# Kernel optimization log

Measured on AMD Instinct MI355X. Metric: run time of the kernel, lower is better.

The kernel has to match this reference:

```python
import jax, jax.numpy as jnp
import numpy as np

NUM_LEVELS = 16
MIN_RES = 16
MAX_RES = 256
LOG2_T = 19
TABLE_SIZE = 1 << LOG2_T
F = 2
N = 262144
HASH_INIT_SCALE = 0.001

# Static constants (mirror the torch buffers)
_PRIMES = np.array([1, 2654435761, 805459861, 3674653429], dtype=np.uint32)
_GROWTH = np.exp((np.log(MAX_RES) - np.log(MIN_RES)) / (NUM_LEVELS - 1))
_SCALINGS = np.floor(MIN_RES * _GROWTH ** np.arange(NUM_LEVELS)).astype(np.float32)  # [L]
_HASH_OFFSET = (np.arange(NUM_LEVELS) * TABLE_SIZE).astype(np.int32)  # [L]
_CORNERS = np.array([[(i >> d) & 1 for d in range(4)] for i in range(16)], dtype=np.int32)  # [16,4]


def setup_inputs() -> dict:
    key = jax.random.key(0)
    k1, k2 = jax.random.split(key)
    xyzt = jax.random.uniform(k1, (N, 4), dtype=jnp.float32)  # coords in [0,1)
    hash_table = (jax.random.uniform(k2, (TABLE_SIZE * NUM_LEVELS, F), dtype=jnp.float32) * 2.0 - 1.0) * HASH_INIT_SCALE
    return {"xyzt": xyzt, "hash_table": hash_table}


def reference(xyzt, hash_table):
    # xyzt: [N,4], hash_table: [L*T, F]
    primes = jnp.asarray(_PRIMES)                      # uint32
    scalings = jnp.asarray(_SCALINGS)                  # [L]
    hash_offset = jnp.asarray(_HASH_OFFSET)            # [L]
    corners = jnp.asarray(_CORNERS)                    # [16,4] int32

    scaled = xyzt[:, None, :] * scalings[None, :, None]          # [N,L,4]
    sf = jnp.floor(scaled)
    offset = scaled - sf                                          # [N,L,4]
    # Coordinates are non-negative, so float->uint32 cast is exact for floor/ceil.
    sf_i = sf.astype(jnp.uint32)
    sc_i = jnp.ceil(scaled).astype(jnp.uint32)

    # [N,L,16,4]: pick ceil where corner bit is 1, else floor
    corner_coords = jnp.where(corners[None, None] == 1, sc_i[:, :, None, :], sf_i[:, :, None, :])

    # Hash: the torch code does (coord_i64 * prime) XOR-reduced, then % 2^19.
    # Since 2^19 divides 2^32, only the low 32 bits matter -> uint32 wraparound
    # multiply + xor + mask gives identical results to the int64 computation.
    mult = corner_coords * primes                                 # uint32 wrap mod 2^32
    h = mult[..., 0] ^ mult[..., 1] ^ mult[..., 2] ^ mult[..., 3]
    idx = (h & jnp.uint32(TABLE_SIZE - 1)).astype(jnp.int32) + hash_offset[None, :, None]  # [N,L,16]

    corner_features = hash_table[idx]                             # [N,L,16,F]

    # Quadrilinear interpolation weights
    w = jnp.where(corners[None, None] == 1, offset[:, :, None, :], 1.0 - offset[:, :, None, :])
    w = jnp.prod(w, axis=-1)                                      # [N,L,16]

    interpolated = jnp.sum(corner_features * w[..., None], axis=2)  # [N,L,F]
    return interpolated.reshape(xyzt.shape[0], NUM_LEVELS * F)
```

## Files before the change

### kernel.cpp

```cpp
#include <hip/hip_runtime.h>
#include <math.h>

#define NUM_LEVELS 16
#define LOG2_T 19
#define TABLE_SIZE (1u << LOG2_T)
#define MASK (TABLE_SIZE - 1u)

struct Scalings { float s[NUM_LEVELS]; };

__global__ __launch_bounds__(256) void hashenc_kernel(
    const float4* __restrict__ xyzt,
    const float2* __restrict__ table,
    float2* __restrict__ dst,
    Scalings sc,
    int n_pts,
    int blocks_per_level,
    int use_scratch)
{
    unsigned b = blockIdx.x;
    unsigned level = b / (unsigned)blocks_per_level;
    unsigned chunk = b - level * (unsigned)blocks_per_level;

    int n = (int)(chunk * 256u + threadIdx.x);
    if (n >= n_pts || level >= NUM_LEVELS) return;

    float4 p = xyzt[n];
    float s = sc.s[level];

    float sx = p.x * s, sy = p.y * s, sz = p.z * s, st = p.w * s;
    float fx = floorf(sx), fy = floorf(sy), fz = floorf(sz), ft = floorf(st);
    float ox = sx - fx, oy = sy - fy, oz = sz - fz, ot = st - ft;

    const unsigned P1 = 2654435761u, P2 = 805459861u, P3 = 3674653429u;
    unsigned xf = (unsigned)fx, xc = (unsigned)ceilf(sx);
    unsigned my_[2] = { (unsigned)fy * P1, (unsigned)ceilf(sy) * P1 };
    unsigned mz_[2] = { (unsigned)fz * P2, (unsigned)ceilf(sz) * P2 };
    unsigned mt_[2] = { (unsigned)ft * P3, (unsigned)ceilf(st) * P3 };
    float wx0 = 1.0f - ox, wx1 = ox;
    float wy_[2] = { 1.0f - oy, oy };
    float wz_[2] = { 1.0f - oz, oz };
    float wt_[2] = { 1.0f - ot, ot };

    unsigned rest[8]; float wrest[8];
    #pragma unroll
    for (int r = 0; r < 8; ++r) {
        rest[r]  = my_[r & 1] ^ mz_[(r >> 1) & 1] ^ mt_[(r >> 2) & 1];
        wrest[r] = wy_[r & 1] * wz_[(r >> 1) & 1] * wt_[(r >> 2) & 1];
    }

    unsigned base = level << LOG2_T;
    float a0 = 0.0f, a1 = 0.0f;

    bool merge = ((xf & 1u) == 0u) && (xc == xf + 1u);
    if (merge) {
        const float4* t4 = (const float4*)table;
        #pragma unroll
        for (int r = 0; r < 8; ++r) {
            unsigned g = ((xf ^ rest[r]) & MASK) + base;
            float4 v = t4[g >> 1];
            bool hi = (g & 1u) != 0u;
            float c0x = hi ? v.z : v.x, c0y = hi ? v.w : v.y;
            float c1x = hi ? v.x : v.z, c1y = hi ? v.y : v.w;
            float wl = wrest[r];
            a0 = fmaf(wl, fmaf(wx0, c0x, wx1 * c1x), a0);
            a1 = fmaf(wl, fmaf(wx0, c0y, wx1 * c1y), a1);
        }
    } else {
        #pragma unroll
        for (int r = 0; r < 8; ++r) {
            unsigned g0 = ((xf ^ rest[r]) & MASK) + base;
            unsigned g1 = ((xc ^ rest[r]) & MASK) + base;
            float2 v0 = table[g0];
            float2 v1 = table[g1];
            float wl = wrest[r];
            a0 = fmaf(wl, fmaf(wx0, v0.x, wx1 * v1.x), a0);
            a1 = fmaf(wl, fmaf(wx0, v0.y, wx1 * v1.y), a1);
        }
    }

    if (use_scratch)
        dst[(size_t)level * n_pts + n] = make_float2(a0, a1);
    else
        dst[(size_t)n * NUM_LEVELS + level] = make_float2(a0, a1);
}

__global__ __launch_bounds__(256) void transpose2_kernel(
    const float4* __restrict__ ws4,
    float4* __restrict__ out,
    int n2)
{
    int t = blockIdx.x * 256 + (int)threadIdx.x;
    if (t >= n2) return;
    float4 v[NUM_LEVELS];
    #pragma unroll
    for (int l = 0; l < NUM_LEVELS; ++l)
        v[l] = ws4[(size_t)l * n2 + t];
    float4* o = out + (size_t)(2 * t) * 8;
    #pragma unroll
    for (int i = 0; i < 8; ++i)
        o[i] = make_float4(v[2 * i].x, v[2 * i].y, v[2 * i + 1].x, v[2 * i + 1].y);
    #pragma unroll
    for (int i = 0; i < 8; ++i)
        o[8 + i] = make_float4(v[2 * i].z, v[2 * i].w, v[2 * i + 1].z, v[2 * i + 1].w);
}

__global__ __launch_bounds__(256) void transpose_kernel(
    const float2* __restrict__ ws,
    float4* __restrict__ out,
    int n_pts)
{
    int n = blockIdx.x * 256 + (int)threadIdx.x;
    if (n >= n_pts) return;
    float2 v[NUM_LEVELS];
    #pragma unroll
    for (int l = 0; l < NUM_LEVELS; ++l)
        v[l] = ws[(size_t)l * n_pts + n];
    float4* o = out + (size_t)n * 8;
    #pragma unroll
    for (int i = 0; i < 8; ++i)
        o[i] = make_float4(v[2 * i].x, v[2 * i].y, v[2 * i + 1].x, v[2 * i + 1].y);
}

extern "C" void kernel_launch(void* const* d_in, const int* in_sizes, int n_in,
                              void* d_out, int out_size, void* d_ws, size_t ws_size,
                              hipStream_t stream) {
    const float4* xyzt  = (const float4*)d_in[0];
    const float2* table = (const float2*)d_in[1];
    int n_pts = in_sizes[0] / 4;

    Scalings sc;
    double growth = exp((log(256.0) - log(16.0)) / 15.0);
    for (int l = 0; l < NUM_LEVELS; ++l)
        sc.s[l] = (float)floor(16.0 * pow(growth, (double)l));

    int block = 256;
    int bpl = (n_pts + block - 1) / block;
    int grid = NUM_LEVELS * bpl;

    size_t need = (size_t)NUM_LEVELS * n_pts * sizeof(float2);
    int use_scratch = (d_ws != nullptr && ws_size >= need) ? 1 : 0;

    float2* dst = use_scratch ? (float2*)d_ws : (float2*)d_out;
    hashenc_kernel<<<grid, block, 0, stream>>>(xyzt, table, dst, sc, n_pts, bpl, use_scratch);

    if (use_scratch) {
        if ((n_pts & 1) == 0) {
            int n2 = n_pts / 2;
            int g2 = (n2 + block - 1) / block;
            transpose2_kernel<<<g2, block, 0, stream>>>((const float4*)d_ws, (float4*)d_out, n2);
        } else {
            transpose_kernel<<<bpl, block, 0, stream>>>((const float2*)d_ws, (float4*)d_out, n_pts);
        }
    }
}
```

Before: 216.9 us.

## Pin hash levels to XCDs and use nontemporal stores for scratch traffic

After: 269.3 us. 1.24x slower.

```diff
diff --git a/kernel.cpp b/kernel.cpp
--- a/kernel.cpp
+++ b/kernel.cpp
@@ -5,6 +5,9 @@
 #define LOG2_T 19
 #define TABLE_SIZE (1u << LOG2_T)
 #define MASK (TABLE_SIZE - 1u)
+
+typedef float vf2 __attribute__((ext_vector_type(2)));
+typedef float vf4 __attribute__((ext_vector_type(4)));
 
 struct Scalings { float s[NUM_LEVELS]; };
 
@@ -14,12 +17,14 @@
     float2* __restrict__ dst,
     Scalings sc,
     int n_pts,
-    int blocks_per_level,
+    int bpl,
     int use_scratch)
 {
     unsigned b = blockIdx.x;
-    unsigned level = b / (unsigned)blocks_per_level;
-    unsigned chunk = b - level * (unsigned)blocks_per_level;
+    unsigned xcd = b & 7u;
+    unsigned slot = b >> 3;
+    unsigned level = (slot < (unsigned)bpl) ? xcd : (15u - xcd);
+    unsigned chunk = (slot < (unsigned)bpl) ? slot : slot - (unsigned)bpl;
 
     int n = (int)(chunk * 256u + threadIdx.x);
     if (n >= n_pts || level >= NUM_LEVELS) return;
@@ -78,30 +83,36 @@
         }
     }
 
-    if (use_scratch)
-        dst[(size_t)level * n_pts + n] = make_float2(a0, a1);
-    else
+    if (use_scratch) {
+        vf2 outv = { a0, a1 };
+        __builtin_nontemporal_store(outv, (vf2*)&dst[(size_t)level * n_pts + n]);
+    } else {
         dst[(size_t)n * NUM_LEVELS + level] = make_float2(a0, a1);
+    }
 }
 
 __global__ __launch_bounds__(256) void transpose2_kernel(
-    const float4* __restrict__ ws4,
-    float4* __restrict__ out,
+    const vf4* __restrict__ ws4,
+    vf4* __restrict__ out,
     int n2)
 {
     int t = blockIdx.x * 256 + (int)threadIdx.x;
     if (t >= n2) return;
-    float4 v[NUM_LEVELS];
+    vf4 v[NUM_LEVELS];
     #pragma unroll
     for (int l = 0; l < NUM_LEVELS; ++l)
-        v[l] = ws4[(size_t)l * n2 + t];
-    float4* o = out + (size_t)(2 * t) * 8;
+        v[l] = __builtin_nontemporal_load(&ws4[(size_t)l * n2 + t]);
+    vf4* o = out + (size_t)(2 * t) * 8;
     #pragma unroll
-    for (int i = 0; i < 8; ++i)
-        o[i] = make_float4(v[2 * i].x, v[2 * i].y, v[2 * i + 1].x, v[2 * i + 1].y);
+    for (int i = 0; i < 8; ++i) {
+        vf4 w = { v[2 * i].x, v[2 * i].y, v[2 * i + 1].x, v[2 * i + 1].y };
+        __builtin_nontemporal_store(w, &o[i]);
+    }
     #pragma unroll
-    for (int i = 0; i < 8; ++i)
-        o[8 + i] = make_float4(v[2 * i].z, v[2 * i].w, v[2 * i + 1].z, v[2 * i + 1].w);
+    for (int i = 0; i < 8; ++i) {
+        vf4 w = { v[2 * i].z, v[2 * i].w, v[2 * i + 1].z, v[2 * i + 1].w };
+        __builtin_nontemporal_store(w, &o[8 + i]);
+    }
 }
 
 __global__ __launch_bounds__(256) void transpose_kernel(
@@ -135,7 +146,7 @@
 
     int block = 256;
     int bpl = (n_pts + block - 1) / block;
-    int grid = NUM_LEVELS * bpl;
+    int grid = 8 * 2 * bpl;
 
     size_t need = (size_t)NUM_LEVELS * n_pts * sizeof(float2);
     int use_scratch = (d_ws != nullptr && ws_size >= need) ? 1 : 0;
@@ -147,7 +158,7 @@
         if ((n_pts & 1) == 0) {
             int n2 = n_pts / 2;
             int g2 = (n2 + block - 1) / block;
-            transpose2_kernel<<<g2, block, 0, stream>>>((const float4*)d_ws, (float4*)d_out, n2);
+            transpose2_kernel<<<g2, block, 0, stream>>>((const vf4*)d_ws, (vf4*)d_out, n2);
         } else {
             transpose_kernel<<<bpl, block, 0, stream>>>((const float2*)d_ws, (float4*)d_out, n_pts);
         }
```
